# Optimization experiments

Measured on AMD Instinct MI355X. Metric: run time of the kernel, lower is better.

Reference implementation:

```python
import jax, jax.numpy as jnp
import numpy as np

GAMMA = 0.99          # discount factor from __init__
TD_LAMBDA = 0.95      # lambda for GAE (lambda < 1 -> GAE branch)
STEP_TYPE_LAST = 2    # alf StepType.LAST


def setup_inputs() -> dict:
    key = jax.random.key(0)
    k0, k1, k2, k3, k4 = jax.random.split(key, 5)
    T1, B = 1024, 4096  # [T+1, B] time-major
    return {
        "value": jax.random.normal(k0, (T1, B), jnp.float32),
        "target_value": jax.random.normal(k1, (T1, B), jnp.float32),
        "reward": jax.random.normal(k2, (T1, B), jnp.float32),
        "step_type": jax.random.randint(k3, (T1, B), 0, 3, jnp.int32),
        "discount": jax.random.uniform(k4, (T1, B), dtype=jnp.float32),
    }


def _gae(reward, target_value, step_type, discount):
    # discounts passed to value_ops are training_info.discount * gamma
    d = discount * GAMMA                                   # [T+1, B]
    is_last = (step_type == STEP_TYPE_LAST).astype(reward.dtype)
    # one-step TD residuals, time-major [T, B]
    delta = reward[1:] + d[1:] * target_value[1:] - target_value[:-1]
    wd = d[1:] * TD_LAMBDA                                 # [T, B]
    not_last = 1.0 - is_last[:-1]                          # [T, B]

    def step(adv_next, xs):
        delta_t, wd_t, nl_t = xs
        adv = nl_t * (delta_t + wd_t * adv_next)
        return adv, adv

    init = jnp.zeros_like(reward[0])                       # [B]
    _, advs = jax.lax.scan(step, init, (delta, wd, not_last), reverse=True)
    return advs                                            # [T, B]


def reference(value, target_value, reward, step_type, discount):
    advs = jax.lax.stop_gradient(_gae(reward, target_value, step_type, discount))
    returns = advs + target_value[:-1]                     # G_t^lambda, [T, B]
    # element_wise_squared_loss(returns.detach(), value[:-1])
    td_err = jax.lax.stop_gradient(returns) - value[:-1]
    loss = td_err * td_err                                 # [T, B]
    # tensor_extend_zero: append a zero row -> [T+1, B]
    return jnp.concatenate([loss, jnp.zeros_like(loss[:1])], axis=0)
```

## Files before the change

### kernel.cpp

```cpp
#include <hip/hip_runtime.h>

#define T      1023
#define B      4096
#define B4     1024
#define CHUNK  16
#define NCHUNK 64

#define GAMMA     0.99f
#define TD_LAMBDA 0.95f

#define COMPOSE_STEP(comp)                                              \
    {                                                                   \
        float d1    = d.comp * GAMMA;                                   \
        float delta = r.comp + d1 * tvn.comp - tvt.comp;                \
        float wd    = d1 * TD_LAMBDA;                                   \
        float nl    = (stt.comp == 2) ? 0.f : 1.f;                      \
        float a     = nl * delta;                                       \
        float bb    = nl * wd;                                          \
        A.comp  = fmaf(bb, A.comp, a);                                  \
        Bf.comp = bb * Bf.comp;                                         \
        tvn.comp = tvt.comp;                                            \
    }

#define REPLAY_STEP(comp)                                               \
    {                                                                   \
        float d1    = d.comp * GAMMA;                                   \
        float delta = r.comp + d1 * tvn.comp - tvt.comp;                \
        float wd    = d1 * TD_LAMBDA;                                   \
        float nl    = (stt.comp == 2) ? 0.f : 1.f;                      \
        adv.comp    = nl * fmaf(wd, adv.comp, delta);                   \
        float td    = adv.comp + tvt.comp - val.comp;                   \
        o.comp      = td * td;                                          \
        tvn.comp    = tvt.comp;                                         \
    }

__global__ __launch_bounds__(256) void k_compose(
    const float4* __restrict__ tv, const float4* __restrict__ rew,
    const int4* __restrict__ st, const float4* __restrict__ disc,
    float4* __restrict__ Ac, float4* __restrict__ Bc)
{
    int tid = blockIdx.x * blockDim.x + threadIdx.x;
    int j = tid & (B4 - 1);
    int c = tid >> 10;
    int s = c * CHUNK;
    int e = min(s + CHUNK, T);

    float4 A  = make_float4(0.f, 0.f, 0.f, 0.f);
    float4 Bf = make_float4(1.f, 1.f, 1.f, 1.f);
    float4 tvn = tv[e * B4 + j];
    for (int t = e - 1; t >= s; --t) {
        int i0 = t * B4 + j;
        int i1 = i0 + B4;
        float4 d   = disc[i1];
        float4 r   = rew[i1];
        int4   stt = st[i0];
        float4 tvt = tv[i0];
        COMPOSE_STEP(x) COMPOSE_STEP(y) COMPOSE_STEP(z) COMPOSE_STEP(w)
    }
    Ac[tid] = A;
    Bc[tid] = Bf;
}

__global__ __launch_bounds__(256) void k_scan(
    const float4* __restrict__ Ac, const float4* __restrict__ Bc,
    float4* __restrict__ R)
{
    int j = blockIdx.x * blockDim.x + threadIdx.x;
    float4 adv = make_float4(0.f, 0.f, 0.f, 0.f);
    for (int c = NCHUNK - 1; c >= 0; --c) {
        int i = c * B4 + j;
        R[i] = adv;
        float4 a = Ac[i], b = Bc[i];
        adv.x = fmaf(b.x, adv.x, a.x);
        adv.y = fmaf(b.y, adv.y, a.y);
        adv.z = fmaf(b.z, adv.z, a.z);
        adv.w = fmaf(b.w, adv.w, a.w);
    }
}

__global__ __launch_bounds__(256) void k_replay(
    const float4* __restrict__ value, const float4* __restrict__ tv,
    const float4* __restrict__ rew, const int4* __restrict__ st,
    const float4* __restrict__ disc, const float4* __restrict__ R,
    float4* __restrict__ out)
{
    int tid = blockIdx.x * blockDim.x + threadIdx.x;
    int j = tid & (B4 - 1);
    int c = tid >> 10;
    int s = c * CHUNK;
    int e = min(s + CHUNK, T);

    float4 adv = R[tid];
    float4 tvn = tv[e * B4 + j];
    if (c == NCHUNK - 1) {
        out[T * B4 + j] = make_float4(0.f, 0.f, 0.f, 0.f);
    }
    for (int t = e - 1; t >= s; --t) {
        int i0 = t * B4 + j;
        int i1 = i0 + B4;
        float4 d   = disc[i1];
        float4 r   = rew[i1];
        int4   stt = st[i0];
        float4 tvt = tv[i0];
        float4 val = value[i0];
        float4 o;
        REPLAY_STEP(x) REPLAY_STEP(y) REPLAY_STEP(z) REPLAY_STEP(w)
        out[i0] = o;
    }
}

extern "C" void kernel_launch(void* const* d_in, const int* in_sizes, int n_in,
                              void* d_out, int out_size, void* d_ws, size_t ws_size,
                              hipStream_t stream) {
    const float4* value = (const float4*)d_in[0];
    const float4* tv    = (const float4*)d_in[1];
    const float4* rew   = (const float4*)d_in[2];
    const int4*   st    = (const int4*)d_in[3];
    const float4* disc  = (const float4*)d_in[4];
    float4* out = (float4*)d_out;

    float4* Ac = (float4*)d_ws;
    float4* Bc = Ac + (size_t)NCHUNK * B4;
    float4* R  = Bc + (size_t)NCHUNK * B4;

    k_compose<<<(NCHUNK * B4) / 256, 256, 0, stream>>>(tv, rew, st, disc, Ac, Bc);
    k_scan<<<B4 / 256, 256, 0, stream>>>(Ac, Bc, R);
    k_replay<<<(NCHUNK * B4) / 256, 256, 0, stream>>>(value, tv, rew, st, disc, R, out);
}
```

Before: 140.6 us.

## Fold inter-chunk carry scan into replay kernel and fully unroll chunk loops

Removes the separate k_scan launch. Each replay thread now recomputes its incoming advantage carry by walking the composed (A,B) pairs of all later chunks in batches of eight. This drops one kernel launch and the R workspace round trip, and lets the scan run in parallel across many threads instead of 16 serial blocks. In exchange, chunk-carry loads grow quadratically in total work, though they are small and cached. The per-chunk time loops are also fully unrolled with a bounds guard so loads can be issued early.

Measured after the change: 134.3 us. -4.5%, faster.

```diff
diff --git a/kernel.cpp b/kernel.cpp
--- a/kernel.cpp
+++ b/kernel.cpp
@@ -9,14 +9,14 @@
 #define GAMMA     0.99f
 #define TD_LAMBDA 0.95f
 
+
 #define COMPOSE_STEP(comp)                                              \
     {                                                                   \
         float d1    = d.comp * GAMMA;                                   \
         float delta = r.comp + d1 * tvn.comp - tvt.comp;                \
-        float wd    = d1 * TD_LAMBDA;                                   \
         float nl    = (stt.comp == 2) ? 0.f : 1.f;                      \
         float a     = nl * delta;                                       \
-        float bb    = nl * wd;                                          \
+        float bb    = nl * (d1 * TD_LAMBDA);                            \
         A.comp  = fmaf(bb, A.comp, a);                                  \
         Bf.comp = bb * Bf.comp;                                         \
         tvn.comp = tvt.comp;                                            \
@@ -26,9 +26,8 @@
     {                                                                   \
         float d1    = d.comp * GAMMA;                                   \
         float delta = r.comp + d1 * tvn.comp - tvt.comp;                \
-        float wd    = d1 * TD_LAMBDA;                                   \
         float nl    = (stt.comp == 2) ? 0.f : 1.f;                      \
-        adv.comp    = nl * fmaf(wd, adv.comp, delta);                   \
+        adv.comp    = nl * fmaf(d1 * TD_LAMBDA, adv.comp, delta);       \
         float td    = adv.comp + tvt.comp - val.comp;                   \
         o.comp      = td * td;                                          \
         tvn.comp    = tvt.comp;                                         \
@@ -39,73 +38,88 @@
     const int4* __restrict__ st, const float4* __restrict__ disc,
     float4* __restrict__ Ac, float4* __restrict__ Bc)
 {
-    int tid = blockIdx.x * blockDim.x + threadIdx.x;
-    int j = tid & (B4 - 1);
-    int c = tid >> 10;
-    int s = c * CHUNK;
-    int e = min(s + CHUNK, T);
+    const int tid = blockIdx.x * 256 + threadIdx.x;
+    const int j = tid & (B4 - 1);
+    const int c = tid >> 10;
+    const int s = c * CHUNK;
+    const int e = min(s + CHUNK, T);
 
     float4 A  = make_float4(0.f, 0.f, 0.f, 0.f);
     float4 Bf = make_float4(1.f, 1.f, 1.f, 1.f);
     float4 tvn = tv[e * B4 + j];
-    for (int t = e - 1; t >= s; --t) {
-        int i0 = t * B4 + j;
-        int i1 = i0 + B4;
-        float4 d   = disc[i1];
-        float4 r   = rew[i1];
-        int4   stt = st[i0];
-        float4 tvt = tv[i0];
-        COMPOSE_STEP(x) COMPOSE_STEP(y) COMPOSE_STEP(z) COMPOSE_STEP(w)
+    #pragma unroll
+    for (int k = CHUNK - 1; k >= 0; --k) {
+        const int t = s + k;
+        if (t < T) {
+            const int i0 = t * B4 + j;
+            const int i1 = i0 + B4;
+            const float4 d   = disc[i1];
+            const float4 r   = rew[i1];
+            const int4   stt = st[i0];
+            const float4 tvt = tv[i0];
+            COMPOSE_STEP(x) COMPOSE_STEP(y) COMPOSE_STEP(z) COMPOSE_STEP(w)
+        }
     }
     Ac[tid] = A;
     Bc[tid] = Bf;
 }
 
-__global__ __launch_bounds__(256) void k_scan(
-    const float4* __restrict__ Ac, const float4* __restrict__ Bc,
-    float4* __restrict__ R)
-{
-    int j = blockIdx.x * blockDim.x + threadIdx.x;
-    float4 adv = make_float4(0.f, 0.f, 0.f, 0.f);
-    for (int c = NCHUNK - 1; c >= 0; --c) {
-        int i = c * B4 + j;
-        R[i] = adv;
-        float4 a = Ac[i], b = Bc[i];
-        adv.x = fmaf(b.x, adv.x, a.x);
-        adv.y = fmaf(b.y, adv.y, a.y);
-        adv.z = fmaf(b.z, adv.z, a.z);
-        adv.w = fmaf(b.w, adv.w, a.w);
-    }
-}
-
 __global__ __launch_bounds__(256) void k_replay(
     const float4* __restrict__ value, const float4* __restrict__ tv,
     const float4* __restrict__ rew, const int4* __restrict__ st,
-    const float4* __restrict__ disc, const float4* __restrict__ R,
+    const float4* __restrict__ disc,
+    const float4* __restrict__ Ac, const float4* __restrict__ Bc,
     float4* __restrict__ out)
 {
-    int tid = blockIdx.x * blockDim.x + threadIdx.x;
-    int j = tid & (B4 - 1);
-    int c = tid >> 10;
-    int s = c * CHUNK;
-    int e = min(s + CHUNK, T);
+    const int tid = blockIdx.x * 256 + threadIdx.x;
+    const int j = tid & (B4 - 1);
+    const int c = tid >> 10;
+    const int s = c * CHUNK;
+    const int e = min(s + CHUNK, T);
 
-    float4 adv = R[tid];
+    float4 adv = make_float4(0.f, 0.f, 0.f, 0.f);
+    int cc = NCHUNK - 1;
+    while (cc > c) {
+        float4 Ab[8], Bb[8];
+        #pragma unroll
+        for (int k = 0; k < 8; ++k) {
+            const int ccc = cc - k;
+            const int i = (ccc > c ? ccc : cc) * B4 + j;
+            Ab[k] = Ac[i];
+            Bb[k] = Bc[i];
+            if (ccc <= c) {
+                Ab[k] = make_float4(0.f, 0.f, 0.f, 0.f);
+                Bb[k] = make_float4(1.f, 1.f, 1.f, 1.f);
+            }
+        }
+        #pragma unroll
+        for (int k = 0; k < 8; ++k) {
+            adv.x = fmaf(Bb[k].x, adv.x, Ab[k].x);
+            adv.y = fmaf(Bb[k].y, adv.y, Ab[k].y);
+            adv.z = fmaf(Bb[k].z, adv.z, Ab[k].z);
+            adv.w = fmaf(Bb[k].w, adv.w, Ab[k].w);
+        }
+        cc -= 8;
+    }
+
     float4 tvn = tv[e * B4 + j];
-    if (c == NCHUNK - 1) {
+    if (c == NCHUNK - 1)
         out[T * B4 + j] = make_float4(0.f, 0.f, 0.f, 0.f);
-    }
-    for (int t = e - 1; t >= s; --t) {
-        int i0 = t * B4 + j;
-        int i1 = i0 + B4;
-        float4 d   = disc[i1];
-        float4 r   = rew[i1];
-        int4   stt = st[i0];
-        float4 tvt = tv[i0];
-        float4 val = value[i0];
-        float4 o;
-        REPLAY_STEP(x) REPLAY_STEP(y) REPLAY_STEP(z) REPLAY_STEP(w)
-        out[i0] = o;
+    #pragma unroll
+    for (int k = CHUNK - 1; k >= 0; --k) {
+        const int t = s + k;
+        if (t < T) {
+            const int i0 = t * B4 + j;
+            const int i1 = i0 + B4;
+            const float4 d   = disc[i1];
+            const float4 r   = rew[i1];
+            const int4   stt = st[i0];
+            const float4 tvt = tv[i0];
+            const float4 val = value[i0];
+            float4 o;
+            REPLAY_STEP(x) REPLAY_STEP(y) REPLAY_STEP(z) REPLAY_STEP(w)
+            out[i0] = o;
+        }
     }
 }
 
@@ -121,9 +135,8 @@
 
     float4* Ac = (float4*)d_ws;
     float4* Bc = Ac + (size_t)NCHUNK * B4;
-    float4* R  = Bc + (size_t)NCHUNK * B4;
 
     k_compose<<<(NCHUNK * B4) / 256, 256, 0, stream>>>(tv, rew, st, disc, Ac, Bc);
-    k_scan<<<B4 / 256, 256, 0, stream>>>(Ac, Bc, R);
-    k_replay<<<(NCHUNK * B4) / 256, 256, 0, stream>>>(value, tv, rew, st, disc, R, out);
+    k_replay<<<(NCHUNK * B4) / 256, 256, 0, stream>>>(value, tv, rew, st, disc,
+                                                      Ac, Bc, out);
 }
```
